# Performance work log

Hardware: AMD Instinct MI355X
Metric: run time of the kernel (lower is better)

Reference implementation:

```python
import jax, jax.numpy as jnp
import numpy as np

B = 256          # batch size
D = 512          # feature_size
P = 5            # num_parts
NC = 11003       # num_classes
SEGC = 6         # segmentation classes
H = 64           # mask spatial size
SCALE = 28.0
ALPHA, BETA = 0.6, 0.4
SP, SN = 10.0, 40.0
TOPK = 8


def _l2n(x, axis):
    return x / jnp.linalg.norm(x, axis=axis, keepdims=True)


def setup_inputs() -> dict:
    key = jax.random.key(0)
    ks = jax.random.split(key, 10)
    return {
        "visual_embed": jax.random.normal(ks[0], (B, D), jnp.float32),
        "textual_embed": jax.random.normal(ks[1], (B, D), jnp.float32),
        "part_embed": jax.random.normal(ks[2], (P, B, D), jnp.float32),
        "attribute_embed": jax.random.normal(ks[3], (P, B, D), jnp.float32),
        "seg_feat": jax.random.normal(ks[4], (B * P, SEGC, H, H), jnp.float32),
        "W": jax.random.normal(ks[5], (D, NC), jnp.float32),
        "labels": jax.random.randint(ks[6], (B,), 0, NC, jnp.int64) if jax.config.jax_enable_x64 else jax.random.randint(ks[6], (B,), 0, NC, jnp.int32),
        "masks": jax.random.randint(ks[7], (B * P, H, H), 0, SEGC, jnp.int32),
        "vmask": jax.random.randint(ks[8], (B, P), 0, 2).astype(bool),
        "tmask": jax.random.randint(ks[9], (B, P), 0, 2).astype(bool),
    }


def _instance_loss(visual_embed, textual_embed, W, labels):
    vn = _l2n(visual_embed, 1)
    tn = _l2n(textual_embed, 1)
    Wn = _l2n(W, 0)
    v_logits = SCALE * (vn @ Wn)          # [B, NC]
    t_logits = SCALE * (tn @ Wn)
    idx = jnp.arange(labels.shape[0])
    v_loss = -jax.nn.log_softmax(v_logits, axis=-1)[idx, labels].mean()
    t_loss = -jax.nn.log_softmax(t_logits, axis=-1)[idx, labels].mean()
    return v_loss + t_loss


def _mask_loss(seg_feat, masks):
    logp = jax.nn.log_softmax(seg_feat, axis=1)                      # [BP, C, H, H]
    ce = -jnp.take_along_axis(logp, masks[:, None, :, :], axis=1)[:, 0]
    return P * ce.mean()


def _global_align_loss(visual_embed, textual_embed, labels):
    vn = _l2n(visual_embed, 1)
    tn = _l2n(textual_embed, 1)
    sim = vn @ tn.T                                                  # [B, B]
    match = labels[:, None] == labels[None, :]
    Lp = jax.nn.softplus(-SP * (sim - ALPHA))
    Ln = jax.nn.softplus(SN * (sim - BETA))
    # original loops over rows then columns, each covering the full matrix
    return 2.0 * jnp.where(match, Lp, Ln).sum() / labels.shape[0]


def _local_align_loss(part_embed, attribute_embed, labels, vmask, tmask):
    pe = _l2n(part_embed, 2)
    ae = _l2n(attribute_embed, 2)
    match = labels[:, None] == labels[None, :]
    bsz = labels.shape[0]
    total = jnp.float32(0.0)
    for i in range(P):  # small fixed loop over parts
        pm = vmask[:, i]
        am = tmask[:, i]
        sim = pe[i] @ ae[i].T                                        # [B, B]
        r1 = jnp.argsort(-sim, axis=1)
        r2 = jnp.argsort(-sim.T, axis=1)
        # NOTE: original code indexes rank1/rank2 with the PART index i
        # (not the sample index j), so the pseudo-label boost is constant
        # across samples within a part; reproduced faithfully.
        fwd1 = r1[i, :TOPK]
        hit1 = (r2[fwd1, :TOPK] == i).any(axis=1)
        boost1 = jnp.zeros(bsz, bool).at[fwd1].set(hit1)
        fwd2 = r2[i, :TOPK]
        hit2 = (r1[fwd2, :TOPK] == i).any(axis=1)
        boost2 = jnp.zeros(bsz, bool).at[fwd2].set(hit2)
        Lp = jax.nn.softplus(-SP * (sim - ALPHA))
        Ln = jax.nn.softplus(SN * (sim - BETA))
        # branch 1: rows j with pm[j], columns k with am[k]
        pos1 = match | boost1[None, :]
        w1 = (pm[:, None] & am[None, :]).astype(sim.dtype)
        b1 = (jnp.where(pos1, Lp, Ln) * w1).sum()
        # branch 2: samples j with pm[j]&am[j], rows k with pm[k]; pred = sim[k, j]
        pos2 = match | boost2[None, :]
        w2 = ((pm & am)[:, None] & pm[None, :]).astype(sim.dtype)
        b2 = (jnp.where(pos2, Lp.T, Ln.T) * w2).sum()
        total = total + (b1 + b2) / bsz
    return total / P


def reference(visual_embed, textual_embed, part_embed, attribute_embed, seg_feat, W,
              labels, masks, vmask, tmask):
    instance_loss = _instance_loss(visual_embed, textual_embed, W, labels)
    mask_loss = _mask_loss(seg_feat, masks)
    global_align_loss = _global_align_loss(visual_embed, textual_embed, labels)
    local_align_loss = _local_align_loss(part_embed, attribute_embed, labels, vmask, tmask)
    return (instance_loss, mask_loss, global_align_loss, local_align_loss)
```

## Files before the change

### kernel.cpp

```cpp
#include <hip/hip_runtime.h>
#include <stdint.h>
#include <stddef.h>

#define BB 256
#define DD 512
#define PP 5
#define NCLS 11003
#define NCP 11008
#define SEGC 6
#define SCALEF 28.0f
#define ALPHAF 0.6f
#define BETAF 0.4f
#define SPF 10.0f
#define SNF 40.0f

typedef __attribute__((ext_vector_type(8))) short bf16x8;
typedef __attribute__((ext_vector_type(4))) float f32x4;

__device__ __forceinline__ float waveSum(float v) {
#pragma unroll
    for (int o = 32; o; o >>= 1) v += __shfl_down(v, o);
    return v;
}

__device__ __forceinline__ float softplusf(float x) {
    return fmaxf(x, 0.f) + log1pf(__expf(-fabsf(x)));
}

__device__ __forceinline__ short to_bf16(float f) {
    uint32_t u = __float_as_uint(f);
    uint32_t r = (u + 0x7FFFu + ((u >> 16) & 1u)) >> 16;
    return (short)r;
}

__global__ __launch_bounds__(256) void convert_k(const void* labels_raw,
                                                 const void* vm_raw,
                                                 const void* tm_raw,
                                                 int* __restrict__ labs,
                                                 unsigned char* __restrict__ vmb,
                                                 unsigned char* __restrict__ tmb) {
    __shared__ int is64, v32, t32;
    if (threadIdx.x == 0) {
        const int* L = (const int*)labels_raw;
        int f = 1;
        for (int j = 0; j < 16; j++) if (L[2 * j + 1] != 0) f = 0;
        is64 = f;
        const int* V = (const int*)vm_raw;
        f = 1;
        for (int j = 0; j < 16; j++) if ((unsigned)V[j] > 1u) f = 0;
        v32 = f;
        const int* T = (const int*)tm_raw;
        f = 1;
        for (int j = 0; j < 16; j++) if ((unsigned)T[j] > 1u) f = 0;
        t32 = f;
    }
    __syncthreads();
    int i = threadIdx.x;
    if (i < BB) {
        if (is64) labs[i] = (int)((const long long*)labels_raw)[i];
        else      labs[i] = ((const int*)labels_raw)[i];
    }
    for (int j = i; j < BB * PP; j += 256) {
        vmb[j] = v32 ? (unsigned char)(((const int*)vm_raw)[j] != 0)
                     : (unsigned char)(((const unsigned char*)vm_raw)[j] != 0);
        tmb[j] = t32 ? (unsigned char)(((const int*)tm_raw)[j] != 0)
                     : (unsigned char)(((const unsigned char*)tm_raw)[j] != 0);
    }
}

__global__ __launch_bounds__(256) void norm_rows_k(const float* __restrict__ src,
                                                   float* __restrict__ dst,
                                                   short* __restrict__ Xp,
                                                   int row_base) {
    int row = blockIdx.x;
    const float* s = src + (size_t)row * DD;
    float v0 = s[threadIdx.x];
    float v1 = s[threadIdx.x + 256];
    float ss = v0 * v0 + v1 * v1;
    __shared__ float red[4];
    __shared__ float inv;
    float v = waveSum(ss);
    if ((threadIdx.x & 63) == 0) red[threadIdx.x >> 6] = v;
    __syncthreads();
    if (threadIdx.x == 0) inv = 1.0f / sqrtf(red[0] + red[1] + red[2] + red[3]);
    __syncthreads();
    float a = v0 * inv, b = v1 * inv;
    float* d = dst + (size_t)row * DD;
    d[threadIdx.x] = a;
    d[threadIdx.x + 256] = b;
    if (Xp) {
        int prow = row_base + row;
        int rt = prow >> 4, rl = prow & 15;
#pragma unroll
        for (int h = 0; h < 2; h++) {
            int c = threadIdx.x + h * 256;
            float val = h ? b : a;
            int kt = c >> 5;
            int lh = (c & 31) >> 3;
            int i = c & 7;
            int lane = (lh << 4) | rl;
            Xp[((size_t)(rt * 16 + kt) * 64 + lane) * 8 + i] = to_bf16(val);
        }
    }
}

__global__ __launch_bounds__(128) void wsq_k(const float* __restrict__ W,
                                             float* __restrict__ swn_sq) {
    int c = blockIdx.x * 128 + threadIdx.x;
    if (c >= NCLS) return;
    int k0 = blockIdx.y * 64;
    float ss = 0.f;
    for (int k = k0; k < k0 + 64; k++) {
        float w = W[(size_t)k * NCLS + c];
        ss = fmaf(w, w, ss);
    }
    atomicAdd(&swn_sq[c], ss);
}

__global__ __launch_bounds__(256) void wtrans_k(const float* __restrict__ W,
                                                short* __restrict__ Wp) {
    __shared__ short tile[32][66];
    int c0 = blockIdx.x * 64, k0 = blockIdx.y * 32;
    int t = threadIdx.x;
    int cl64 = t & 63, kl = t >> 6;
#pragma unroll
    for (int it = 0; it < 8; it++) {
        int k = k0 + kl + it * 4;
        int c = c0 + cl64;
        float w = (c < NCLS) ? W[(size_t)k * NCLS + c] : 0.f;
        tile[kl + it * 4][cl64] = to_bf16(w);
    }
    __syncthreads();
    int ctl = t >> 6, lane = t & 63;
    int cl = lane & 15, lh = lane >> 4;
    bf16x8 v;
#pragma unroll
    for (int i = 0; i < 8; i++) v[i] = tile[lh * 8 + i][ctl * 16 + cl];
    int ct = blockIdx.x * 4 + ctl;
    *(bf16x8*)(Wp + ((size_t)(ct * 16 + blockIdx.y) * 64 + lane) * 8) = v;
}

__global__ __launch_bounds__(256) void logits_mfma_k(const short* __restrict__ Xp,
                                                     const short* __restrict__ Wp,
                                                     const float* __restrict__ swn_sq,
                                                     float* __restrict__ sumexp) {
    int wave = threadIdx.x >> 6;
    int lane = threadIdx.x & 63;
    int l15 = lane & 15, lh = lane >> 4;
    int rt = blockIdx.y * 4 + wave;
    int ct0 = blockIdx.x * 4;
    f32x4 acc0 = {0.f, 0.f, 0.f, 0.f};
    f32x4 acc1 = acc0, acc2 = acc0, acc3 = acc0;
    const short* ap = Xp + (size_t)rt * 16 * 64 * 8 + lane * 8;
    const short* bp = Wp + (size_t)ct0 * 16 * 64 * 8 + lane * 8;
#pragma unroll
    for (int kt = 0; kt < 16; kt++) {
        bf16x8 a  = *(const bf16x8*)(ap + (size_t)kt * 512);
        bf16x8 b0 = *(const bf16x8*)(bp + (size_t)kt * 512);
        bf16x8 b1 = *(const bf16x8*)(bp + (size_t)(16 * 512) + kt * 512);
        bf16x8 b2 = *(const bf16x8*)(bp + (size_t)(32 * 512) + kt * 512);
        bf16x8 b3 = *(const bf16x8*)(bp + (size_t)(48 * 512) + kt * 512);
        acc0 = __builtin_amdgcn_mfma_f32_16x16x32_bf16(a, b0, acc0, 0, 0, 0);
        acc1 = __builtin_amdgcn_mfma_f32_16x16x32_bf16(a, b1, acc1, 0, 0, 0);
        acc2 = __builtin_amdgcn_mfma_f32_16x16x32_bf16(a, b2, acc2, 0, 0, 0);
        acc3 = __builtin_amdgcn_mfma_f32_16x16x32_bf16(a, b3, acc3, 0, 0, 0);
    }
    float s0 = 0.f, s1 = 0.f, s2 = 0.f, s3 = 0.f;
#pragma unroll
    for (int j = 0; j < 4; j++) {
        int c = (ct0 + j) * 16 + l15;
        bool valid = c < NCLS;
        float sc = valid ? SCALEF / sqrtf(swn_sq[c]) : 0.f;
        f32x4 accj = (j == 0) ? acc0 : (j == 1) ? acc1 : (j == 2) ? acc2 : acc3;
        s0 += valid ? __expf(accj[0] * sc) : 0.f;
        s1 += valid ? __expf(accj[1] * sc) : 0.f;
        s2 += valid ? __expf(accj[2] * sc) : 0.f;
        s3 += valid ? __expf(accj[3] * sc) : 0.f;
    }
#pragma unroll
    for (int o = 1; o < 16; o <<= 1) {
        s0 += __shfl_xor(s0, o);
        s1 += __shfl_xor(s1, o);
        s2 += __shfl_xor(s2, o);
        s3 += __shfl_xor(s3, o);
    }
    if (l15 == 0) {
        int rbase = rt * 16 + 4 * lh;
        atomicAdd(&sumexp[rbase + 0], s0);
        atomicAdd(&sumexp[rbase + 1], s1);
        atomicAdd(&sumexp[rbase + 2], s2);
        atomicAdd(&sumexp[rbase + 3], s3);
    }
}

__global__ __launch_bounds__(256) void inst_label_k(const float* __restrict__ Xn,
                                                    const float* __restrict__ W,
                                                    const float* __restrict__ swn_sq,
                                                    const float* __restrict__ sumexp,
                                                    const int* __restrict__ labs,
                                                    double* __restrict__ iacc) {
    int i = blockIdx.x;
    int t = threadIdx.x;
    int lab = labs[i];
    float dv = 0.f, dt_ = 0.f;
    for (int k = t; k < DD; k += 256) {
        float w = W[(size_t)k * NCLS + lab];
        dv = fmaf(Xn[(size_t)i * DD + k], w, dv);
        dt_ = fmaf(Xn[(size_t)(BB + i) * DD + k], w, dt_);
    }
    __shared__ float rv[4], rt[4];
    float a = waveSum(dv), b = waveSum(dt_);
    if ((t & 63) == 0) { rv[t >> 6] = a; rt[t >> 6] = b; }
    __syncthreads();
    if (t == 0) {
        float sc = SCALEF / sqrtf(swn_sq[lab]);
        float dvs = (rv[0] + rv[1] + rv[2] + rv[3]) * sc;
        float dts = (rt[0] + rt[1] + rt[2] + rt[3]) * sc;
        float li = (logf(sumexp[i]) - dvs) + (logf(sumexp[BB + i]) - dts);
        atomicAdd(iacc, (double)li);
    }
}

__global__ __launch_bounds__(256) void mask_loss_k(const float* __restrict__ seg,
                                                   const int* __restrict__ masks,
                                                   double* __restrict__ acc) {
    int idx = blockIdx.x * 256 + threadIdx.x;
    int n = idx >> 12;
    int pix = idx & 4095;
    const float* p = seg + (size_t)n * SEGC * 4096 + pix;
    float x0 = p[0], x1 = p[4096], x2 = p[8192];
    float x3 = p[12288], x4 = p[16384], x5 = p[20480];
    float mx = fmaxf(fmaxf(fmaxf(x0, x1), fmaxf(x2, x3)), fmaxf(x4, x5));
    float se = __expf(x0 - mx) + __expf(x1 - mx) + __expf(x2 - mx) +
               __expf(x3 - mx) + __expf(x4 - mx) + __expf(x5 - mx);
    int m = masks[idx];
    float xm = (m == 0) ? x0 : (m == 1) ? x1 : (m == 2) ? x2
             : (m == 3) ? x3 : (m == 4) ? x4 : x5;
    float ce = logf(se) + mx - xm;
    __shared__ float red[4];
    float v = waveSum(ce);
    if ((threadIdx.x & 63) == 0) red[threadIdx.x >> 6] = v;
    __syncthreads();
    if (threadIdx.x == 0)
        atomicAdd(&acc[blockIdx.x & 63], (double)(red[0] + red[1] + red[2] + red[3]));
}

__global__ __launch_bounds__(256) void sim_k(const float* __restrict__ vn,
                                             const float* __restrict__ tn,
                                             const float* __restrict__ pn,
                                             const float* __restrict__ an,
                                             float* __restrict__ sims) {
    int z = blockIdx.z;
    const float* X;
    const float* Y;
    if (z == 0) { X = vn; Y = tn; }
    else { X = pn + (size_t)(z - 1) * BB * DD; Y = an + (size_t)(z - 1) * BB * DD; }
    float* C = sims + (size_t)z * BB * BB;
    int row0 = blockIdx.y * 32, col0 = blockIdx.x * 32;
    int tx = threadIdx.x & 15, ty = threadIdx.x >> 4;
    __shared__ float Xs[32][33], Ys[32][33];
    float a00 = 0, a01 = 0, a10 = 0, a11 = 0;
    for (int kc = 0; kc < DD; kc += 32) {
#pragma unroll
        for (int l = 0; l < 4; l++) {
            int idx = threadIdx.x + l * 256;
            int r = idx >> 5, kk = idx & 31;
            Xs[r][kk] = X[(size_t)(row0 + r) * DD + kc + kk];
            Ys[r][kk] = Y[(size_t)(col0 + r) * DD + kc + kk];
        }
        __syncthreads();
#pragma unroll
        for (int kk = 0; kk < 32; kk++) {
            float x0 = Xs[ty * 2][kk], x1 = Xs[ty * 2 + 1][kk];
            float y0 = Ys[tx * 2][kk], y1 = Ys[tx * 2 + 1][kk];
            a00 = fmaf(x0, y0, a00);
            a01 = fmaf(x0, y1, a01);
            a10 = fmaf(x1, y0, a10);
            a11 = fmaf(x1, y1, a11);
        }
        __syncthreads();
    }
    int r = row0 + ty * 2, c = col0 + tx * 2;
    C[(size_t)r * BB + c] = a00;
    C[(size_t)r * BB + c + 1] = a01;
    C[(size_t)(r + 1) * BB + c] = a10;
    C[(size_t)(r + 1) * BB + c + 1] = a11;
}

__global__ __launch_bounds__(256) void boost_k(const float* __restrict__ sims,
                                               unsigned char* __restrict__ b1,
                                               unsigned char* __restrict__ b2) {
    int i = blockIdx.x;
    const float* S = sims + (size_t)(i + 1) * BB * BB;
    int c = threadIdx.x;
    __shared__ float rowv[BB], colv[BB];
    rowv[c] = S[(size_t)i * BB + c];
    colv[c] = S[(size_t)c * BB + i];
    __syncthreads();
    float rv = rowv[c], cv = colv[c];
    int rank1 = 0, rank2 = 0;
    for (int j = 0; j < BB; j++) {
        rank1 += rowv[j] > rv;
        rank2 += colv[j] > cv;
    }
    unsigned char bo1 = 0, bo2 = 0;
    if (rank1 < 8) {
        int cnt = 0;
        for (int a = 0; a < BB; a++) cnt += S[(size_t)a * BB + c] > rv;
        bo1 = (cnt < 8);
    }
    if (rank2 < 8) {
        int cnt = 0;
        for (int b = 0; b < BB; b++) cnt += S[(size_t)c * BB + b] > cv;
        bo2 = (cnt < 8);
    }
    b1[i * BB + c] = bo1;
    b2[i * BB + c] = bo2;
}

__global__ __launch_bounds__(256) void galign_k(const float* __restrict__ sim,
                                                const int* __restrict__ labs,
                                                double* __restrict__ acc) {
    int r = blockIdx.x, c = threadIdx.x;
    float s = sim[(size_t)r * BB + c];
    float x = (labs[r] == labs[c]) ? (-SPF * (s - ALPHAF)) : (SNF * (s - BETAF));
    float v = softplusf(x);
    __shared__ float red[4];
    v = waveSum(v);
    if ((threadIdx.x & 63) == 0) red[threadIdx.x >> 6] = v;
    __syncthreads();
    if (threadIdx.x == 0)
        atomicAdd(&acc[blockIdx.x & 7], (double)(red[0] + red[1] + red[2] + red[3]));
}

__global__ __launch_bounds__(256) void lalign_k(const float* __restrict__ sims,
                                                const int* __restrict__ labs,
                                                const unsigned char* __restrict__ vmb,
                                                const unsigned char* __restrict__ tmb,
                                                const unsigned char* __restrict__ b1,
                                                const unsigned char* __restrict__ b2,
                                                double* __restrict__ acc) {
    int i = blockIdx.y, r = blockIdx.x, c = threadIdx.x;
    const float* S = sims + (size_t)(i + 1) * BB * BB;
    float s = S[(size_t)r * BB + c];
    bool m = labs[r] == labs[c];
    float Lp = softplusf(-SPF * (s - ALPHAF));
    float Ln = softplusf(SNF * (s - BETAF));
    bool pmr = vmb[r * PP + i] != 0;
    bool pmc = vmb[c * PP + i] != 0;
    bool amc = tmb[c * PP + i] != 0;
    float v = 0.f;
    if (pmr && amc) v += (m || (b1[i * BB + c] != 0)) ? Lp : Ln;
    if (pmc && amc && pmr) v += (m || (b2[i * BB + r] != 0)) ? Lp : Ln;
    __shared__ float red[4];
    v = waveSum(v);
    if ((threadIdx.x & 63) == 0) red[threadIdx.x >> 6] = v;
    __syncthreads();
    if (threadIdx.x == 0)
        atomicAdd(&acc[blockIdx.x & 7], (double)(red[0] + red[1] + red[2] + red[3]));
}

__global__ void finalize_k(const double* __restrict__ accs, float* __restrict__ out) {
    int t = threadIdx.x;
    double mv = accs[t];
    double gv = (t < 8) ? accs[64 + t] : 0.0;
    double lv = (t < 8) ? accs[72 + t] : 0.0;
#pragma unroll
    for (int o = 32; o; o >>= 1) {
        mv += __shfl_down(mv, o);
        gv += __shfl_down(gv, o);
        lv += __shfl_down(lv, o);
    }
    if (t == 0) {
        out[0] = (float)(accs[80] / (double)BB);
        out[1] = (float)((double)PP * mv / 5242880.0);
        out[2] = (float)(2.0 * gv / (double)BB);
        out[3] = (float)(lv / (double)(BB * PP));
    }
}

extern "C" void kernel_launch(void* const* d_in, const int* in_sizes, int n_in,
                              void* d_out, int out_size, void* d_ws, size_t ws_size,
                              hipStream_t stream) {
    const float* visual  = (const float*)d_in[0];
    const float* textual = (const float*)d_in[1];
    const float* part    = (const float*)d_in[2];
    const float* attr    = (const float*)d_in[3];
    const float* seg     = (const float*)d_in[4];
    const float* W       = (const float*)d_in[5];
    const void*  labels  = d_in[6];
    const int*   masks   = (const int*)d_in[7];
    const void*  vmask   = d_in[8];
    const void*  tmask   = d_in[9];
    float* out = (float*)d_out;

    float* ws = (float*)d_ws;
    short* Wp   = (short*)ws;
    float* base = ws + (size_t)NCP * DD / 2;
    short* Xp   = (short*)base;
    float* vn   = base + (size_t)BB * DD;
    float* tn   = vn + (size_t)BB * DD;
    float* pn   = tn + (size_t)BB * DD;
    float* an   = pn + (size_t)PP * BB * DD;
    float* swn_sq = an + (size_t)PP * BB * DD;
    float* sims = swn_sq + NCP;
    float* sumexp = sims + 6 * BB * BB;
    int* labs = (int*)(sumexp + 2 * BB);
    unsigned char* vmb = (unsigned char*)(labs + BB);
    unsigned char* tmb = vmb + BB * PP;
    unsigned char* b1  = tmb + BB * PP;
    unsigned char* b2  = b1 + BB * PP;
    uintptr_t aaddr = ((uintptr_t)(b2 + BB * PP) + 15) & ~(uintptr_t)15;
    double* accs = (double*)aaddr;

    hipMemsetAsync(sumexp, 0, 2 * BB * sizeof(float), stream);
    hipMemsetAsync(swn_sq, 0, NCP * sizeof(float), stream);
    hipMemsetAsync(accs, 0, 81 * sizeof(double), stream);

    convert_k<<<1, 256, 0, stream>>>(labels, vmask, tmask, labs, vmb, tmb);

    norm_rows_k<<<BB, 256, 0, stream>>>(visual, vn, Xp, 0);
    norm_rows_k<<<BB, 256, 0, stream>>>(textual, tn, Xp, BB);
    norm_rows_k<<<PP * BB, 256, 0, stream>>>(part, pn, nullptr, 0);
    norm_rows_k<<<PP * BB, 256, 0, stream>>>(attr, an, nullptr, 0);

    dim3 wg(86, 8);
    wsq_k<<<wg, 128, 0, stream>>>(W, swn_sq);
    dim3 tg(NCP / 64, 16);
    wtrans_k<<<tg, 256, 0, stream>>>(W, Wp);

    dim3 mg(NCP / 64, 8);
    logits_mfma_k<<<mg, 256, 0, stream>>>(Xp, Wp, swn_sq, sumexp);
    inst_label_k<<<BB, 256, 0, stream>>>(vn, W, swn_sq, sumexp, labs, accs + 80);

    mask_loss_k<<<5242880 / 256, 256, 0, stream>>>(seg, masks, accs);

    dim3 sg(8, 8, 6);
    sim_k<<<sg, 256, 0, stream>>>(vn, tn, pn, an, sims);
    boost_k<<<PP, 256, 0, stream>>>(sims, b1, b2);

    galign_k<<<BB, 256, 0, stream>>>(sims, labs, accs + 64);
    dim3 lg(BB, PP);
    lalign_k<<<lg, 256, 0, stream>>>(sims, labs, vmb, tmb, b1, b2, accs + 72);

    finalize_k<<<1, 64, 0, stream>>>(accs, out);
}
```

Measured before the change: 386.7 us.

## Fuse column norms into W transpose, vectorize mask loss, merge align kernels

```diff
diff --git a/kernel.cpp b/kernel.cpp
--- a/kernel.cpp
+++ b/kernel.cpp
@@ -104,32 +104,26 @@
     }
 }
 
-__global__ __launch_bounds__(128) void wsq_k(const float* __restrict__ W,
-                                             float* __restrict__ swn_sq) {
-    int c = blockIdx.x * 128 + threadIdx.x;
-    if (c >= NCLS) return;
-    int k0 = blockIdx.y * 64;
-    float ss = 0.f;
-    for (int k = k0; k < k0 + 64; k++) {
-        float w = W[(size_t)k * NCLS + c];
-        ss = fmaf(w, w, ss);
-    }
-    atomicAdd(&swn_sq[c], ss);
-}
-
 __global__ __launch_bounds__(256) void wtrans_k(const float* __restrict__ W,
-                                                short* __restrict__ Wp) {
+                                                short* __restrict__ Wp,
+                                                float* __restrict__ swn_sq) {
     __shared__ short tile[32][66];
+    __shared__ float colsum[64];
     int c0 = blockIdx.x * 64, k0 = blockIdx.y * 32;
     int t = threadIdx.x;
+    if (t < 64) colsum[t] = 0.f;
+    __syncthreads();
     int cl64 = t & 63, kl = t >> 6;
+    float ss = 0.f;
 #pragma unroll
     for (int it = 0; it < 8; it++) {
         int k = k0 + kl + it * 4;
         int c = c0 + cl64;
         float w = (c < NCLS) ? W[(size_t)k * NCLS + c] : 0.f;
+        ss = fmaf(w, w, ss);
         tile[kl + it * 4][cl64] = to_bf16(w);
     }
+    atomicAdd(&colsum[cl64], ss);
     __syncthreads();
     int ctl = t >> 6, lane = t & 63;
     int cl = lane & 15, lh = lane >> 4;
@@ -138,6 +132,7 @@
     for (int i = 0; i < 8; i++) v[i] = tile[lh * 8 + i][ctl * 16 + cl];
     int ct = blockIdx.x * 4 + ctl;
     *(bf16x8*)(Wp + ((size_t)(ct * 16 + blockIdx.y) * 64 + lane) * 8) = v;
+    if (t < 64) atomicAdd(&swn_sq[c0 + t], colsum[t]);
 }
 
 __global__ __launch_bounds__(256) void logits_mfma_k(const short* __restrict__ Xp,
@@ -224,21 +219,36 @@
 __global__ __launch_bounds__(256) void mask_loss_k(const float* __restrict__ seg,
                                                    const int* __restrict__ masks,
                                                    double* __restrict__ acc) {
-    int idx = blockIdx.x * 256 + threadIdx.x;
-    int n = idx >> 12;
-    int pix = idx & 4095;
-    const float* p = seg + (size_t)n * SEGC * 4096 + pix;
-    float x0 = p[0], x1 = p[4096], x2 = p[8192];
-    float x3 = p[12288], x4 = p[16384], x5 = p[20480];
-    float mx = fmaxf(fmaxf(fmaxf(x0, x1), fmaxf(x2, x3)), fmaxf(x4, x5));
-    float se = __expf(x0 - mx) + __expf(x1 - mx) + __expf(x2 - mx) +
-               __expf(x3 - mx) + __expf(x4 - mx) + __expf(x5 - mx);
-    int m = masks[idx];
-    float xm = (m == 0) ? x0 : (m == 1) ? x1 : (m == 2) ? x2
-             : (m == 3) ? x3 : (m == 4) ? x4 : x5;
-    float ce = logf(se) + mx - xm;
+    int tid = blockIdx.x * 256 + threadIdx.x;
+    int n = tid >> 10;
+    int q = (tid & 1023) << 2;
+    const float* p = seg + (size_t)n * (SEGC * 4096) + q;
+    float4 x0 = *(const float4*)(p);
+    float4 x1 = *(const float4*)(p + 4096);
+    float4 x2 = *(const float4*)(p + 8192);
+    float4 x3 = *(const float4*)(p + 12288);
+    float4 x4 = *(const float4*)(p + 16384);
+    float4 x5 = *(const float4*)(p + 20480);
+    int4 mm = *(const int4*)(masks + (size_t)n * 4096 + q);
+    float tot = 0.f;
+#pragma unroll
+    for (int j = 0; j < 4; j++) {
+        float a0 = ((const float*)&x0)[j];
+        float a1 = ((const float*)&x1)[j];
+        float a2 = ((const float*)&x2)[j];
+        float a3 = ((const float*)&x3)[j];
+        float a4 = ((const float*)&x4)[j];
+        float a5 = ((const float*)&x5)[j];
+        int m = ((const int*)&mm)[j];
+        float mx = fmaxf(fmaxf(fmaxf(a0, a1), fmaxf(a2, a3)), fmaxf(a4, a5));
+        float se = __expf(a0 - mx) + __expf(a1 - mx) + __expf(a2 - mx) +
+                   __expf(a3 - mx) + __expf(a4 - mx) + __expf(a5 - mx);
+        float xm = (m == 0) ? a0 : (m == 1) ? a1 : (m == 2) ? a2
+                 : (m == 3) ? a3 : (m == 4) ? a4 : a5;
+        tot += logf(se) + mx - xm;
+    }
     __shared__ float red[4];
-    float v = waveSum(ce);
+    float v = waveSum(tot);
     if ((threadIdx.x & 63) == 0) red[threadIdx.x >> 6] = v;
     __syncthreads();
     if (threadIdx.x == 0)
@@ -318,46 +328,40 @@
     b2[i * BB + c] = bo2;
 }
 
-__global__ __launch_bounds__(256) void galign_k(const float* __restrict__ sim,
-                                                const int* __restrict__ labs,
-                                                double* __restrict__ acc) {
-    int r = blockIdx.x, c = threadIdx.x;
-    float s = sim[(size_t)r * BB + c];
-    float x = (labs[r] == labs[c]) ? (-SPF * (s - ALPHAF)) : (SNF * (s - BETAF));
-    float v = softplusf(x);
-    __shared__ float red[4];
-    v = waveSum(v);
-    if ((threadIdx.x & 63) == 0) red[threadIdx.x >> 6] = v;
-    __syncthreads();
-    if (threadIdx.x == 0)
-        atomicAdd(&acc[blockIdx.x & 7], (double)(red[0] + red[1] + red[2] + red[3]));
-}
-
 __global__ __launch_bounds__(256) void lalign_k(const float* __restrict__ sims,
                                                 const int* __restrict__ labs,
                                                 const unsigned char* __restrict__ vmb,
                                                 const unsigned char* __restrict__ tmb,
                                                 const unsigned char* __restrict__ b1,
                                                 const unsigned char* __restrict__ b2,
-                                                double* __restrict__ acc) {
+                                                double* __restrict__ accL,
+                                                double* __restrict__ accG) {
     int i = blockIdx.y, r = blockIdx.x, c = threadIdx.x;
-    const float* S = sims + (size_t)(i + 1) * BB * BB;
-    float s = S[(size_t)r * BB + c];
-    bool m = labs[r] == labs[c];
-    float Lp = softplusf(-SPF * (s - ALPHAF));
-    float Ln = softplusf(SNF * (s - BETAF));
-    bool pmr = vmb[r * PP + i] != 0;
-    bool pmc = vmb[c * PP + i] != 0;
-    bool amc = tmb[c * PP + i] != 0;
     float v = 0.f;
-    if (pmr && amc) v += (m || (b1[i * BB + c] != 0)) ? Lp : Ln;
-    if (pmc && amc && pmr) v += (m || (b2[i * BB + r] != 0)) ? Lp : Ln;
+    if (i == PP) {
+        float s = sims[(size_t)r * BB + c];
+        float x = (labs[r] == labs[c]) ? (-SPF * (s - ALPHAF)) : (SNF * (s - BETAF));
+        v = softplusf(x);
+    } else {
+        const float* S = sims + (size_t)(i + 1) * BB * BB;
+        float s = S[(size_t)r * BB + c];
+        bool m = labs[r] == labs[c];
+        float Lp = softplusf(-SPF * (s - ALPHAF));
+        float Ln = softplusf(SNF * (s - BETAF));
+        bool pmr = vmb[r * PP + i] != 0;
+        bool pmc = vmb[c * PP + i] != 0;
+        bool amc = tmb[c * PP + i] != 0;
+        if (pmr && amc) v += (m || (b1[i * BB + c] != 0)) ? Lp : Ln;
+        if (pmc && amc && pmr) v += (m || (b2[i * BB + r] != 0)) ? Lp : Ln;
+    }
     __shared__ float red[4];
     v = waveSum(v);
     if ((threadIdx.x & 63) == 0) red[threadIdx.x >> 6] = v;
     __syncthreads();
-    if (threadIdx.x == 0)
-        atomicAdd(&acc[blockIdx.x & 7], (double)(red[0] + red[1] + red[2] + red[3]));
+    if (threadIdx.x == 0) {
+        double* dst = (i == PP) ? &accG[r & 7] : &accL[r & 7];
+        atomicAdd(dst, (double)(red[0] + red[1] + red[2] + red[3]));
+    }
 }
 
 __global__ void finalize_k(const double* __restrict__ accs, float* __restrict__ out) {
@@ -424,24 +428,21 @@
     norm_rows_k<<<PP * BB, 256, 0, stream>>>(part, pn, nullptr, 0);
     norm_rows_k<<<PP * BB, 256, 0, stream>>>(attr, an, nullptr, 0);
 
-    dim3 wg(86, 8);
-    wsq_k<<<wg, 128, 0, stream>>>(W, swn_sq);
     dim3 tg(NCP / 64, 16);
-    wtrans_k<<<tg, 256, 0, stream>>>(W, Wp);
+    wtrans_k<<<tg, 256, 0, stream>>>(W, Wp, swn_sq);
 
     dim3 mg(NCP / 64, 8);
     logits_mfma_k<<<mg, 256, 0, stream>>>(Xp, Wp, swn_sq, sumexp);
     inst_label_k<<<BB, 256, 0, stream>>>(vn, W, swn_sq, sumexp, labs, accs + 80);
 
-    mask_loss_k<<<5242880 / 256, 256, 0, stream>>>(seg, masks, accs);
+    mask_loss_k<<<1310720 / 256, 256, 0, stream>>>(seg, masks, accs);
 
     dim3 sg(8, 8, 6);
     sim_k<<<sg, 256, 0, stream>>>(vn, tn, pn, an, sims);
     boost_k<<<PP, 256, 0, stream>>>(sims, b1, b2);
 
-    galign_k<<<BB, 256, 0, stream>>>(sims, labs, accs + 64);
-    dim3 lg(BB, PP);
-    lalign_k<<<lg, 256, 0, stream>>>(sims, labs, vmb, tmb, b1, b2, accs + 72);
+    dim3 lg(BB, PP + 1);
+    lalign_k<<<lg, 256, 0, stream>>>(sims, labs, vmb, tmb, b1, b2, accs + 72, accs + 64);
 
     finalize_k<<<1, 64, 0, stream>>>(accs, out);
 }
```

After: 373.2 us. 3.5% less time.
